# Kernel optimization log

Measured on AMD Instinct MI355X. Metric: run time of the kernel, lower is better.

## Reference

```python
import jax, jax.numpy as jnp
import numpy as np

N_HEADS = 16
ROPE_BASE = 10000.0

def apply_rope(x):
    # x: [B, H, S, D] with D even; interleaved-pair RoPE (torchtune style)
    B, H, S, D = x.shape
    half = D // 2
    inv_freq = 1.0 / (ROPE_BASE ** (jnp.arange(0, half, dtype=jnp.float32) / half))
    angles = jnp.arange(S, dtype=jnp.float32)[:, None] * inv_freq[None, :]  # [S, D/2]
    cos = jnp.cos(angles)[None, None]  # [1,1,S,D/2]
    sin = jnp.sin(angles)[None, None]
    x1 = x[..., 0::2]
    x2 = x[..., 1::2]
    r1 = x1 * cos - x2 * sin
    r2 = x1 * sin + x2 * cos
    return jnp.stack([r1, r2], axis=-1).reshape(B, H, S, D)

def setup_inputs() -> dict:
    key = jax.random.key(0)
    ks = jax.random.split(key, 5)
    B, S, E = 2, 2048, 1024
    d_attn = 1024
    scale = 1.0 / np.sqrt(E)
    x = jax.random.normal(ks[0], (B, S, E), dtype=jnp.float32)
    Wq = jax.random.normal(ks[1], (d_attn, E), dtype=jnp.float32) * scale
    Wk = jax.random.normal(ks[2], (d_attn, E), dtype=jnp.float32) * scale
    Wv = jax.random.normal(ks[3], (d_attn, E), dtype=jnp.float32) * scale
    Wo = jax.random.normal(ks[4], (E, d_attn), dtype=jnp.float32) * scale
    return {"x": x, "Wq": Wq, "Wk": Wk, "Wv": Wv, "Wo": Wo}

def reference(x, Wq, Wk, Wv, Wo):
    B, S, E = x.shape
    d_attn = Wq.shape[0]
    hd = d_attn // N_HEADS
    attn_scale = 1.0 / np.sqrt(d_attn)
    # projections (nn.Linear: x @ W.T), split heads -> [B, H, S, hd]
    q = (x @ Wq.T).reshape(B, S, N_HEADS, hd).transpose(0, 2, 1, 3)
    k = (x @ Wk.T).reshape(B, S, N_HEADS, hd).transpose(0, 2, 1, 3)
    v = (x @ Wv.T).reshape(B, S, N_HEADS, hd).transpose(0, 2, 1, 3)
    q = apply_rope(q)
    k = apply_rope(k)
    scores = jnp.einsum('bhqd,bhkd->bhqk', q, k) * attn_scale  # [B,H,S,S]
    causal = jnp.tril(jnp.ones((S, S), dtype=bool))
    scores = jnp.where(causal[None, None], scores, -jnp.inf)
    probs = jax.nn.softmax(scores, axis=-1)  # dropout is identity in eval
    out = jnp.einsum('bhqk,bhkd->bhqd', probs, v)
    out = out.transpose(0, 2, 1, 3).reshape(B, S, d_attn)
    return out @ Wo.T
```

## Files before the change

### kernel.cpp

```cpp
#include <hip/hip_runtime.h>


typedef float  f32x4  __attribute__((ext_vector_type(4)));
typedef short  short8 __attribute__((ext_vector_type(8)));

#define MFMA16(a,b,c) __builtin_amdgcn_mfma_f32_16x16x32_bf16((a),(b),(c),0,0,0)
#define GLD_LDS16(g, l)                                                        \
  __builtin_amdgcn_global_load_lds(                                            \
      (const __attribute__((address_space(1))) unsigned int*)(g),              \
      (__attribute__((address_space(3))) unsigned int*)(l), 16, 0, 0)

__device__ __forceinline__ unsigned short f2bf(float f) {
  unsigned int x = __float_as_uint(f);
  x += 0x7fffu + ((x >> 16) & 1u);
  return (unsigned short)(x >> 16);
}
__device__ __forceinline__ float bf2f(unsigned short u) {
  return __uint_as_float(((unsigned int)u) << 16);
}

__global__ __launch_bounds__(256) void cvt_all(const float* __restrict__ x,
                                               const float* __restrict__ wq,
                                               const float* __restrict__ wk,
                                               const float* __restrict__ wv,
                                               const float* __restrict__ wo,
                                               ushort* __restrict__ dst) {
  const int i = blockIdx.x * 256 + threadIdx.x;
  const float* src;
  int off;
  if (i < 1048576) { src = x; off = i; }
  else {
    const int j = i - 1048576;
    const int wsel = j >> 18;
    off = j & 262143;
    src = (wsel == 0) ? wq : (wsel == 1) ? wk : (wsel == 2) ? wv : wo;
  }
  const float4 v = ((const float4*)src)[off];
  ushort4 o = make_ushort4(f2bf(v.x), f2bf(v.y), f2bf(v.z), f2bf(v.w));
  ((ushort4*)dst)[i] = o;
}

template<int MODE>
__global__ __launch_bounds__(256) void gemm_bt(const ushort* __restrict__ A,
                                               const ushort* __restrict__ B,
                                               void* __restrict__ Cv,
                                               int K) {
  __shared__ __align__(16) short As[128 * 32];
  __shared__ __align__(16) short Bs[128 * 32];
  const int tid  = threadIdx.x;
  const int lane = tid & 63, w = tid >> 6;
  const int ln   = lane & 15, quad = lane >> 4;
  const int wm   = w >> 1, wn = w & 1;
  const int m0 = blockIdx.y * 128, n0 = blockIdx.x * 128;

  const int srow = lane >> 2;
  const int schk = (lane & 3) * 8;
  const ushort* Ag0 = A + (size_t)(m0 + w * 32      + srow) * K + schk;
  const ushort* Ag1 = A + (size_t)(m0 + w * 32 + 16 + srow) * K + schk;
  const ushort* Bg0 = B + (size_t)(n0 + w * 32      + srow) * K + schk;
  const ushort* Bg1 = B + (size_t)(n0 + w * 32 + 16 + srow) * K + schk;
  short* lA0 = As + (w * 32) * 32;
  short* lA1 = As + (w * 32 + 16) * 32;
  short* lB0 = Bs + (w * 32) * 32;
  short* lB1 = Bs + (w * 32 + 16) * 32;

  int aoff[4], boff[4];
#pragma unroll
  for (int i = 0; i < 4; i++) {
    aoff[i] = (wm * 64 + i * 16 + ln) * 32 + quad * 8;
    boff[i] = (wn * 64 + i * 16 + ln) * 32 + quad * 8;
  }
  f32x4 acc[4][4] = {};

  for (int kt = 0; kt < K; kt += 32) {
    __syncthreads();
    GLD_LDS16(Ag0 + kt, lA0);
    GLD_LDS16(Ag1 + kt, lA1);
    GLD_LDS16(Bg0 + kt, lB0);
    GLD_LDS16(Bg1 + kt, lB1);
    __syncthreads();
    short8 av[4], bv[4];
#pragma unroll
    for (int i = 0; i < 4; i++) av[i] = *(const short8*)&As[aoff[i]];
#pragma unroll
    for (int i = 0; i < 4; i++) bv[i] = *(const short8*)&Bs[boff[i]];
#pragma unroll
    for (int mi = 0; mi < 4; mi++)
#pragma unroll
      for (int ni = 0; ni < 4; ni++)
        acc[mi][ni] = MFMA16(av[mi], bv[ni], acc[mi][ni]);
  }

  if (MODE == 0) {
    ushort* Cq = (ushort*)Cv;
    if (n0 < 2048) {
      ushort* dst = Cq + (n0 < 1024 ? 0 : 4194304);
      const int nbase = (n0 < 1024) ? n0 : n0 - 1024;
#pragma unroll
      for (int mi = 0; mi < 4; mi++) {
        const int row = m0 + wm * 64 + mi * 16 + quad * 4;
#pragma unroll
        for (int ni = 0; ni < 4; ni++) {
          const int col = nbase + wn * 64 + ni * 16 + ln;
#pragma unroll
          for (int r = 0; r < 4; r++)
            dst[(size_t)(row + r) * 1024 + col] = f2bf(acc[mi][ni][r]);
        }
      }
    } else {
      ushort* vt = Cq + 8388608;
#pragma unroll
      for (int mi = 0; mi < 4; mi++) {
        const int sm = m0 + wm * 64 + mi * 16 + quad * 4;
        const int b = sm >> 11, s = sm & 2047;
#pragma unroll
        for (int ni = 0; ni < 4; ni++) {
          const int nv = (n0 - 2048) + wn * 64 + ni * 16 + ln;
          const int bh = b * 16 + (nv >> 6), d = nv & 63;
          ushort4 u = make_ushort4(f2bf(acc[mi][ni][0]), f2bf(acc[mi][ni][1]),
                                   f2bf(acc[mi][ni][2]), f2bf(acc[mi][ni][3]));
          *(ushort4*)&vt[((size_t)bh * 64 + d) * 2048 + s] = u;
        }
      }
    }
  } else {
    float* C = (float*)Cv;
#pragma unroll
    for (int mi = 0; mi < 4; mi++) {
      const int row = m0 + wm * 64 + mi * 16 + quad * 4;
#pragma unroll
      for (int ni = 0; ni < 4; ni++) {
        const int col = n0 + wn * 64 + ni * 16 + ln;
#pragma unroll
        for (int r = 0; r < 4; r++)
          C[(size_t)(row + r) * 1024 + col] = acc[mi][ni][r];
      }
    }
  }
}

__global__ __launch_bounds__(256) void ropek(ushort* __restrict__ qk) {
  const int g  = blockIdx.x * 256 + threadIdx.x;
  const int P0 = g << 2;
  const int mv = P0 >> 9;
  const int s  = mv & 2047;
  const int i0 = P0 & 31;
  const float scale = (mv < 4096) ? 0.04508422002778011f : 1.0f;
  short8 u = *(short8*)&qk[(size_t)P0 * 2];
  short8 ov;
#pragma unroll
  for (int t = 0; t < 4; t++) {
    const float invf = expf(-(float)(i0 + t) * 0.28782313662425574f);
    const float ang  = (float)s * invf;
    float sn, cs;
    sincosf(ang, &sn, &cs);
    const float x1 = bf2f((unsigned short)u[2 * t]);
    const float x2 = bf2f((unsigned short)u[2 * t + 1]);
    ov[2 * t]     = (short)f2bf((x1 * cs - x2 * sn) * scale);
    ov[2 * t + 1] = (short)f2bf((x1 * sn + x2 * cs) * scale);
  }
  *(short8*)&qk[(size_t)P0 * 2] = ov;
}

__global__ __launch_bounds__(256) void attnk(const ushort* __restrict__ q,
                                             const ushort* __restrict__ k,
                                             const ushort* __restrict__ vt,
                                             ushort* __restrict__ ctx) {
  __shared__ __align__(16) short Ks[64 * 72];
  __shared__ __align__(16) short Vs[64 * 72];
  __shared__ __align__(16) short Ps[4 * 16 * 72];
  const int tid  = threadIdx.x;
  const int lane = tid & 63, w = tid >> 6;
  const int ln   = lane & 15, quad = lane >> 4;
  const int x = blockIdx.x, bh = blockIdx.y;
  const int b = bh >> 4, h = bh & 15;
  const int jA = x, jB = 31 - x;
  short* Pw = Ps + w * 1152;

  const size_t qbA = ((size_t)(b * 2048 + jA * 64 + w * 16 + ln)) * 1024 + h * 64;
  const size_t qbB = ((size_t)(b * 2048 + jB * 64 + w * 16 + ln)) * 1024 + h * 64;
  const short8 aqA0 = *(const short8*)&q[qbA + quad * 8];
  const short8 aqA1 = *(const short8*)&q[qbA + 32 + quad * 8];
  const short8 aqB0 = *(const short8*)&q[qbB + quad * 8];
  const short8 aqB1 = *(const short8*)&q[qbB + 32 + quad * 8];

  f32x4 oA[4] = {}, oB[4] = {};
  float lsA[4] = {0.f, 0.f, 0.f, 0.f}, lsB[4] = {0.f, 0.f, 0.f, 0.f};

  const int s0 = tid, s1 = tid + 256;
  const int r0 = s0 >> 3, c0 = (s0 & 7) * 8;
  const int r1 = s1 >> 3, c1 = (s1 & 7) * 8;
  const ushort* kg0 = k  + ((size_t)(b * 2048 + r0)) * 1024 + h * 64 + c0;
  const ushort* kg1 = k  + ((size_t)(b * 2048 + r1)) * 1024 + h * 64 + c1;
  const ushort* vg0 = vt + ((size_t)(bh * 64 + r0)) * 2048 + c0;
  const ushort* vg1 = vt + ((size_t)(bh * 64 + r1)) * 2048 + c1;
  const int wK0 = r0 * 72 + c0, wK1 = r1 * 72 + c1;

  for (int t = 0; t <= jB; t++) {
    __syncthreads();
    *(short8*)&Ks[wK0] = *(const short8*)(kg0 + (size_t)t * 65536);
    *(short8*)&Ks[wK1] = *(const short8*)(kg1 + (size_t)t * 65536);
    *(short8*)&Vs[wK0] = *(const short8*)(vg0 + t * 64);
    *(short8*)&Vs[wK1] = *(const short8*)(vg1 + t * 64);
    __syncthreads();

    const bool actA = (t <= jA);
    f32x4 scA[4], scB[4];
#pragma unroll
    for (int ct = 0; ct < 4; ct++) {
      const short8 bk0 = *(const short8*)&Ks[(ct * 16 + ln) * 72 + quad * 8];
      const short8 bk1 = *(const short8*)&Ks[(ct * 16 + ln) * 72 + 32 + quad * 8];
      f32x4 z = {0.f, 0.f, 0.f, 0.f};
      z = MFMA16(aqB0, bk0, z);
      z = MFMA16(aqB1, bk1, z);
      scB[ct] = z;
      if (actA) {
        f32x4 y = {0.f, 0.f, 0.f, 0.f};
        y = MFMA16(aqA0, bk0, y);
        y = MFMA16(aqA1, bk1, y);
        scA[ct] = y;
      }
    }
    if (t == jB) {
#pragma unroll
      for (int ct = 0; ct < 4; ct++) {
        const int kv = (t << 6) + ct * 16 + ln;
#pragma unroll
        for (int r = 0; r < 4; r++)
          if (kv > jB * 64 + w * 16 + quad * 4 + r) scB[ct][r] = -100000.0f;
      }
    }
    if (actA && t == jA) {
#pragma unroll
      for (int ct = 0; ct < 4; ct++) {
        const int kv = (t << 6) + ct * 16 + ln;
#pragma unroll
        for (int r = 0; r < 4; r++)
          if (kv > jA * 64 + w * 16 + quad * 4 + r) scA[ct][r] = -100000.0f;
      }
    }

    short8 bv0[4], bv1[4];
#pragma unroll
    for (int dt = 0; dt < 4; dt++) {
      bv0[dt] = *(const short8*)&Vs[(dt * 16 + ln) * 72 + quad * 8];
      bv1[dt] = *(const short8*)&Vs[(dt * 16 + ln) * 72 + 32 + quad * 8];
    }

#pragma unroll
    for (int ct = 0; ct < 4; ct++)
#pragma unroll
      for (int r = 0; r < 4; r++) {
        const float p = __builtin_amdgcn_exp2f(scB[ct][r]);
        lsB[r] += p;
        Pw[(quad * 4 + r) * 72 + ct * 16 + ln] = (short)f2bf(p);
      }
    {
      const short8 ap0 = *(const short8*)&Pw[ln * 72 + quad * 8];
      const short8 ap1 = *(const short8*)&Pw[ln * 72 + 32 + quad * 8];
#pragma unroll
      for (int dt = 0; dt < 4; dt++) {
        oB[dt] = MFMA16(ap0, bv0[dt], oB[dt]);
        oB[dt] = MFMA16(ap1, bv1[dt], oB[dt]);
      }
    }
    if (actA) {
#pragma unroll
      for (int ct = 0; ct < 4; ct++)
#pragma unroll
        for (int r = 0; r < 4; r++) {
          const float p = __builtin_amdgcn_exp2f(scA[ct][r]);
          lsA[r] += p;
          Pw[(quad * 4 + r) * 72 + ct * 16 + ln] = (short)f2bf(p);
        }
      const short8 ap0 = *(const short8*)&Pw[ln * 72 + quad * 8];
      const short8 ap1 = *(const short8*)&Pw[ln * 72 + 32 + quad * 8];
#pragma unroll
      for (int dt = 0; dt < 4; dt++) {
        oA[dt] = MFMA16(ap0, bv0[dt], oA[dt]);
        oA[dt] = MFMA16(ap1, bv1[dt], oA[dt]);
      }
    }
  }

#pragma unroll
  for (int off = 1; off < 16; off <<= 1)
#pragma unroll
    for (int r = 0; r < 4; r++) {
      lsA[r] += __shfl_xor(lsA[r], off, 64);
      lsB[r] += __shfl_xor(lsB[r], off, 64);
    }

#pragma unroll
  for (int r = 0; r < 4; r++) {
    const float invA = 1.0f / lsA[r];
    const float invB = 1.0f / lsB[r];
    const int rowA = jA * 64 + w * 16 + quad * 4 + r;
    const int rowB = jB * 64 + w * 16 + quad * 4 + r;
#pragma unroll
    for (int dt = 0; dt < 4; dt++) {
      ctx[((size_t)(b * 2048 + rowA)) * 1024 + h * 64 + dt * 16 + ln] =
          f2bf(oA[dt][r] * invA);
      ctx[((size_t)(b * 2048 + rowB)) * 1024 + h * 64 + dt * 16 + ln] =
          f2bf(oB[dt][r] * invB);
    }
  }
}

extern "C" void kernel_launch(void* const* d_in, const int* in_sizes, int n_in,
                              void* d_out, int out_size, void* d_ws, size_t ws_size,
                              hipStream_t stream) {
  const float* x  = (const float*)d_in[0];
  const float* Wq = (const float*)d_in[1];
  const float* Wk = (const float*)d_in[2];
  const float* Wv = (const float*)d_in[3];
  const float* Wo = (const float*)d_in[4];
  float* out = (float*)d_out;
  char* ws = (char*)d_ws;

  ushort* xb  = (ushort*)(ws);
  ushort* wqb = (ushort*)(ws + (size_t)(8  << 20));
  ushort* qb  = (ushort*)(ws + (size_t)(16 << 20));
  ushort* kb  = (ushort*)(ws + (size_t)(24 << 20));
  ushort* vtb = (ushort*)(ws + (size_t)(32 << 20));
  ushort* ctx = (ushort*)(ws + (size_t)(40 << 20));

  cvt_all<<<8192, 256, 0, stream>>>(x, Wq, Wk, Wv, Wo, xb);
  gemm_bt<0><<<dim3(24, 32), 256, 0, stream>>>(xb, wqb, (void*)qb, 1024);
  ropek<<<4096, 256, 0, stream>>>(qb);
  attnk<<<dim3(16, 32), 256, 0, stream>>>(qb, kb, vtb, ctx);
  gemm_bt<2><<<dim3(8, 32), 256, 0, stream>>>(ctx, wqb + 3145728 , (void*)out, 1024);
}
```

Measured before the change: 205.9 us.

## Split attention KV loop across two wave groups, narrow output GEMM tiles, fast RoPE trig

The attention kernel now runs 512 threads per block. Two groups of four waves each process alternating KV tiles, and their partial outputs and row sums are merged through shared memory at the end, so each block's serial causal loop is roughly half as long. The output projection GEMM uses 64-wide N tiles, which doubles its grid and gives more blocks across the CUs. RoPE switches from expf/sincosf to hardware exp2/sin/cos with explicit range reduction to revolutions, trading a little accuracy for cheaper trig. The cost is a larger shared-memory footprint and an extra reduction step per attention block.

After: 230.7 us. 1.12x slower.

```diff
diff --git a/kernel.cpp b/kernel.cpp
--- a/kernel.cpp
+++ b/kernel.cpp
@@ -40,54 +40,57 @@
   ((ushort4*)dst)[i] = o;
 }
 
-template<int MODE>
+template<int MODE, int BN>
 __global__ __launch_bounds__(256) void gemm_bt(const ushort* __restrict__ A,
                                                const ushort* __restrict__ B,
                                                void* __restrict__ Cv,
                                                int K) {
+  constexpr int NI = BN / 32;
   __shared__ __align__(16) short As[128 * 32];
-  __shared__ __align__(16) short Bs[128 * 32];
+  __shared__ __align__(16) short Bs[BN * 32];
   const int tid  = threadIdx.x;
   const int lane = tid & 63, w = tid >> 6;
   const int ln   = lane & 15, quad = lane >> 4;
   const int wm   = w >> 1, wn = w & 1;
-  const int m0 = blockIdx.y * 128, n0 = blockIdx.x * 128;
+  const int m0 = blockIdx.y * 128, n0 = blockIdx.x * BN;
 
   const int srow = lane >> 2;
   const int schk = (lane & 3) * 8;
   const ushort* Ag0 = A + (size_t)(m0 + w * 32      + srow) * K + schk;
   const ushort* Ag1 = A + (size_t)(m0 + w * 32 + 16 + srow) * K + schk;
-  const ushort* Bg0 = B + (size_t)(n0 + w * 32      + srow) * K + schk;
-  const ushort* Bg1 = B + (size_t)(n0 + w * 32 + 16 + srow) * K + schk;
+  const int brow = (BN == 128) ? w * 32 : w * 16;
+  const ushort* Bg0 = B + (size_t)(n0 + brow + srow) * K + schk;
+  const ushort* Bg1 = B + (size_t)(n0 + brow + 16 + srow) * K + schk;
   short* lA0 = As + (w * 32) * 32;
   short* lA1 = As + (w * 32 + 16) * 32;
-  short* lB0 = Bs + (w * 32) * 32;
-  short* lB1 = Bs + (w * 32 + 16) * 32;
-
-  int aoff[4], boff[4];
-#pragma unroll
-  for (int i = 0; i < 4; i++) {
+  short* lB0 = Bs + brow * 32;
+  short* lB1 = Bs + (brow + 16) * 32;
+
+  int aoff[4], boff[NI];
+#pragma unroll
+  for (int i = 0; i < 4; i++)
     aoff[i] = (wm * 64 + i * 16 + ln) * 32 + quad * 8;
-    boff[i] = (wn * 64 + i * 16 + ln) * 32 + quad * 8;
-  }
-  f32x4 acc[4][4] = {};
+#pragma unroll
+  for (int i = 0; i < NI; i++)
+    boff[i] = (wn * (BN / 2) + i * 16 + ln) * 32 + quad * 8;
+  f32x4 acc[4][NI] = {};
 
   for (int kt = 0; kt < K; kt += 32) {
     __syncthreads();
     GLD_LDS16(Ag0 + kt, lA0);
     GLD_LDS16(Ag1 + kt, lA1);
     GLD_LDS16(Bg0 + kt, lB0);
-    GLD_LDS16(Bg1 + kt, lB1);
+    if (BN == 128) GLD_LDS16(Bg1 + kt, lB1);
     __syncthreads();
-    short8 av[4], bv[4];
+    short8 av[4], bv[NI];
 #pragma unroll
     for (int i = 0; i < 4; i++) av[i] = *(const short8*)&As[aoff[i]];
 #pragma unroll
-    for (int i = 0; i < 4; i++) bv[i] = *(const short8*)&Bs[boff[i]];
+    for (int i = 0; i < NI; i++) bv[i] = *(const short8*)&Bs[boff[i]];
 #pragma unroll
     for (int mi = 0; mi < 4; mi++)
 #pragma unroll
-      for (int ni = 0; ni < 4; ni++)
+      for (int ni = 0; ni < NI; ni++)
         acc[mi][ni] = MFMA16(av[mi], bv[ni], acc[mi][ni]);
   }
 
@@ -100,8 +103,8 @@
       for (int mi = 0; mi < 4; mi++) {
         const int row = m0 + wm * 64 + mi * 16 + quad * 4;
 #pragma unroll
-        for (int ni = 0; ni < 4; ni++) {
-          const int col = nbase + wn * 64 + ni * 16 + ln;
+        for (int ni = 0; ni < NI; ni++) {
+          const int col = nbase + wn * (BN / 2) + ni * 16 + ln;
 #pragma unroll
           for (int r = 0; r < 4; r++)
             dst[(size_t)(row + r) * 1024 + col] = f2bf(acc[mi][ni][r]);
@@ -114,8 +117,8 @@
         const int sm = m0 + wm * 64 + mi * 16 + quad * 4;
         const int b = sm >> 11, s = sm & 2047;
 #pragma unroll
-        for (int ni = 0; ni < 4; ni++) {
-          const int nv = (n0 - 2048) + wn * 64 + ni * 16 + ln;
+        for (int ni = 0; ni < NI; ni++) {
+          const int nv = (n0 - 2048) + wn * (BN / 2) + ni * 16 + ln;
           const int bh = b * 16 + (nv >> 6), d = nv & 63;
           ushort4 u = make_ushort4(f2bf(acc[mi][ni][0]), f2bf(acc[mi][ni][1]),
                                    f2bf(acc[mi][ni][2]), f2bf(acc[mi][ni][3]));
@@ -129,8 +132,8 @@
     for (int mi = 0; mi < 4; mi++) {
       const int row = m0 + wm * 64 + mi * 16 + quad * 4;
 #pragma unroll
-      for (int ni = 0; ni < 4; ni++) {
-        const int col = n0 + wn * 64 + ni * 16 + ln;
+      for (int ni = 0; ni < NI; ni++) {
+        const int col = n0 + wn * (BN / 2) + ni * 16 + ln;
 #pragma unroll
         for (int r = 0; r < 4; r++)
           C[(size_t)(row + r) * 1024 + col] = acc[mi][ni][r];
@@ -146,14 +149,16 @@
   const int s  = mv & 2047;
   const int i0 = P0 & 31;
   const float scale = (mv < 4096) ? 0.04508422002778011f : 1.0f;
+  const float sf = (float)s;
   short8 u = *(short8*)&qk[(size_t)P0 * 2];
   short8 ov;
 #pragma unroll
   for (int t = 0; t < 4; t++) {
-    const float invf = expf(-(float)(i0 + t) * 0.28782313662425574f);
-    const float ang  = (float)s * invf;
-    float sn, cs;
-    sincosf(ang, &sn, &cs);
+    const float invf = __builtin_amdgcn_exp2f(-(float)(i0 + t) * 0.4152410118579865f);
+    const float rev  = sf * invf * 0.15915494309189535f;
+    const float rr   = rev - floorf(rev);
+    const float sn = __builtin_amdgcn_sinf(rr);
+    const float cs = __builtin_amdgcn_cosf(rr);
     const float x1 = bf2f((unsigned short)u[2 * t]);
     const float x2 = bf2f((unsigned short)u[2 * t + 1]);
     ov[2 * t]     = (short)f2bf((x1 * cs - x2 * sn) * scale);
@@ -162,23 +167,31 @@
   *(short8*)&qk[(size_t)P0 * 2] = ov;
 }
 
-__global__ __launch_bounds__(256) void attnk(const ushort* __restrict__ q,
-                                             const ushort* __restrict__ k,
-                                             const ushort* __restrict__ vt,
-                                             ushort* __restrict__ ctx) {
-  __shared__ __align__(16) short Ks[64 * 72];
-  __shared__ __align__(16) short Vs[64 * 72];
-  __shared__ __align__(16) short Ps[4 * 16 * 72];
+__global__ __launch_bounds__(512, 4) void attnk(const ushort* __restrict__ q,
+                                                const ushort* __restrict__ k,
+                                                const ushort* __restrict__ vt,
+                                                ushort* __restrict__ ctx) {
+  __shared__ __align__(16) char smem[55296];
+  short* KsB = (short*)smem;
+  short* VsB = (short*)(smem + 18432);
+  short* PsB = (short*)(smem + 36864);
+  float* OcA = (float*)smem;
+  float* OcB = (float*)(smem + 16384);
+  float* Lc  = (float*)(smem + 32768);
+
   const int tid  = threadIdx.x;
   const int lane = tid & 63, w = tid >> 6;
-  const int ln   = lane & 15, quad = lane >> 4;
+  const int g = w >> 2, wg = w & 3;
+  const int ln = lane & 15, quad = lane >> 4;
   const int x = blockIdx.x, bh = blockIdx.y;
   const int b = bh >> 4, h = bh & 15;
   const int jA = x, jB = 31 - x;
-  short* Pw = Ps + w * 1152;
-
-  const size_t qbA = ((size_t)(b * 2048 + jA * 64 + w * 16 + ln)) * 1024 + h * 64;
-  const size_t qbB = ((size_t)(b * 2048 + jB * 64 + w * 16 + ln)) * 1024 + h * 64;
+  short* Ks = KsB + g * 4608;
+  short* Vs = VsB + g * 4608;
+  short* Pw = PsB + w * 1152;
+
+  const size_t qbA = ((size_t)(b * 2048 + jA * 64 + wg * 16 + ln)) * 1024 + h * 64;
+  const size_t qbB = ((size_t)(b * 2048 + jB * 64 + wg * 16 + ln)) * 1024 + h * 64;
   const short8 aqA0 = *(const short8*)&q[qbA + quad * 8];
   const short8 aqA1 = *(const short8*)&q[qbA + 32 + quad * 8];
   const short8 aqB0 = *(const short8*)&q[qbB + quad * 8];
@@ -187,98 +200,104 @@
   f32x4 oA[4] = {}, oB[4] = {};
   float lsA[4] = {0.f, 0.f, 0.f, 0.f}, lsB[4] = {0.f, 0.f, 0.f, 0.f};
 
-  const int s0 = tid, s1 = tid + 256;
-  const int r0 = s0 >> 3, c0 = (s0 & 7) * 8;
-  const int r1 = s1 >> 3, c1 = (s1 & 7) * 8;
+  const int tg = tid & 255;
+  const int r0 = tg >> 3, c0 = (tg & 7) * 8;
+  const int r1 = r0 + 32, c1 = c0;
   const ushort* kg0 = k  + ((size_t)(b * 2048 + r0)) * 1024 + h * 64 + c0;
   const ushort* kg1 = k  + ((size_t)(b * 2048 + r1)) * 1024 + h * 64 + c1;
   const ushort* vg0 = vt + ((size_t)(bh * 64 + r0)) * 2048 + c0;
   const ushort* vg1 = vt + ((size_t)(bh * 64 + r1)) * 2048 + c1;
   const int wK0 = r0 * 72 + c0, wK1 = r1 * 72 + c1;
 
-  for (int t = 0; t <= jB; t++) {
+  const int nsteps = (jB >> 1) + 1;
+  for (int i = 0; i < nsteps; ++i) {
+    const int t = 2 * i + g;
+    const bool act = (t <= jB);
     __syncthreads();
-    *(short8*)&Ks[wK0] = *(const short8*)(kg0 + (size_t)t * 65536);
-    *(short8*)&Ks[wK1] = *(const short8*)(kg1 + (size_t)t * 65536);
-    *(short8*)&Vs[wK0] = *(const short8*)(vg0 + t * 64);
-    *(short8*)&Vs[wK1] = *(const short8*)(vg1 + t * 64);
+    if (act) {
+      *(short8*)&Ks[wK0] = *(const short8*)(kg0 + (size_t)t * 65536);
+      *(short8*)&Ks[wK1] = *(const short8*)(kg1 + (size_t)t * 65536);
+      *(short8*)&Vs[wK0] = *(const short8*)(vg0 + t * 64);
+      *(short8*)&Vs[wK1] = *(const short8*)(vg1 + t * 64);
+    }
     __syncthreads();
-
-    const bool actA = (t <= jA);
-    f32x4 scA[4], scB[4];
-#pragma unroll
-    for (int ct = 0; ct < 4; ct++) {
-      const short8 bk0 = *(const short8*)&Ks[(ct * 16 + ln) * 72 + quad * 8];
-      const short8 bk1 = *(const short8*)&Ks[(ct * 16 + ln) * 72 + 32 + quad * 8];
-      f32x4 z = {0.f, 0.f, 0.f, 0.f};
-      z = MFMA16(aqB0, bk0, z);
-      z = MFMA16(aqB1, bk1, z);
-      scB[ct] = z;
+    if (act) {
+      const bool actA = (t <= jA);
+      f32x4 scA[4], scB[4];
+#pragma unroll
+      for (int ct = 0; ct < 4; ct++) {
+        const short8 bk0 = *(const short8*)&Ks[(ct * 16 + ln) * 72 + quad * 8];
+        const short8 bk1 = *(const short8*)&Ks[(ct * 16 + ln) * 72 + 32 + quad * 8];
+        f32x4 z = {0.f, 0.f, 0.f, 0.f};
+        z = MFMA16(aqB0, bk0, z);
+        z = MFMA16(aqB1, bk1, z);
+        scB[ct] = z;
+        if (actA) {
+          f32x4 y = {0.f, 0.f, 0.f, 0.f};
+          y = MFMA16(aqA0, bk0, y);
+          y = MFMA16(aqA1, bk1, y);
+          scA[ct] = y;
+        }
+      }
+      if (t == jB) {
+#pragma unroll
+        for (int ct = 0; ct < 4; ct++) {
+          const int kv = (t << 6) + ct * 16 + ln;
+#pragma unroll
+          for (int r = 0; r < 4; r++)
+            if (kv > jB * 64 + wg * 16 + quad * 4 + r) scB[ct][r] = -100000.0f;
+        }
+      }
+      if (actA && t == jA) {
+#pragma unroll
+        for (int ct = 0; ct < 4; ct++) {
+          const int kv = (t << 6) + ct * 16 + ln;
+#pragma unroll
+          for (int r = 0; r < 4; r++)
+            if (kv > jA * 64 + wg * 16 + quad * 4 + r) scA[ct][r] = -100000.0f;
+        }
+      }
+
+      short8 bv0[4], bv1[4];
+#pragma unroll
+      for (int dt = 0; dt < 4; dt++) {
+        bv0[dt] = *(const short8*)&Vs[(dt * 16 + ln) * 72 + quad * 8];
+        bv1[dt] = *(const short8*)&Vs[(dt * 16 + ln) * 72 + 32 + quad * 8];
+      }
+
+#pragma unroll
+      for (int ct = 0; ct < 4; ct++)
+#pragma unroll
+        for (int r = 0; r < 4; r++) {
+          const float p = __builtin_amdgcn_exp2f(scB[ct][r]);
+          lsB[r] += p;
+          Pw[(quad * 4 + r) * 72 + ct * 16 + ln] = (short)f2bf(p);
+        }
+      {
+        const short8 ap0 = *(const short8*)&Pw[ln * 72 + quad * 8];
+        const short8 ap1 = *(const short8*)&Pw[ln * 72 + 32 + quad * 8];
+#pragma unroll
+        for (int dt = 0; dt < 4; dt++) {
+          oB[dt] = MFMA16(ap0, bv0[dt], oB[dt]);
+          oB[dt] = MFMA16(ap1, bv1[dt], oB[dt]);
+        }
+      }
       if (actA) {
-        f32x4 y = {0.f, 0.f, 0.f, 0.f};
-        y = MFMA16(aqA0, bk0, y);
-        y = MFMA16(aqA1, bk1, y);
-        scA[ct] = y;
-      }
-    }
-    if (t == jB) {
-#pragma unroll
-      for (int ct = 0; ct < 4; ct++) {
-        const int kv = (t << 6) + ct * 16 + ln;
-#pragma unroll
-        for (int r = 0; r < 4; r++)
-          if (kv > jB * 64 + w * 16 + quad * 4 + r) scB[ct][r] = -100000.0f;
-      }
-    }
-    if (actA && t == jA) {
-#pragma unroll
-      for (int ct = 0; ct < 4; ct++) {
-        const int kv = (t << 6) + ct * 16 + ln;
-#pragma unroll
-        for (int r = 0; r < 4; r++)
-          if (kv > jA * 64 + w * 16 + quad * 4 + r) scA[ct][r] = -100000.0f;
-      }
-    }
-
-    short8 bv0[4], bv1[4];
-#pragma unroll
-    for (int dt = 0; dt < 4; dt++) {
-      bv0[dt] = *(const short8*)&Vs[(dt * 16 + ln) * 72 + quad * 8];
-      bv1[dt] = *(const short8*)&Vs[(dt * 16 + ln) * 72 + 32 + quad * 8];
-    }
-
-#pragma unroll
-    for (int ct = 0; ct < 4; ct++)
-#pragma unroll
-      for (int r = 0; r < 4; r++) {
-        const float p = __builtin_amdgcn_exp2f(scB[ct][r]);
-        lsB[r] += p;
-        Pw[(quad * 4 + r) * 72 + ct * 16 + ln] = (short)f2bf(p);
-      }
-    {
-      const short8 ap0 = *(const short8*)&Pw[ln * 72 + quad * 8];
-      const short8 ap1 = *(const short8*)&Pw[ln * 72 + 32 + quad * 8];
-#pragma unroll
-      for (int dt = 0; dt < 4; dt++) {
-        oB[dt] = MFMA16(ap0, bv0[dt], oB[dt]);
-        oB[dt] = MFMA16(ap1, bv1[dt], oB[dt]);
-      }
-    }
-    if (actA) {
-#pragma unroll
-      for (int ct = 0; ct < 4; ct++)
-#pragma unroll
-        for (int r = 0; r < 4; r++) {
-          const float p = __builtin_amdgcn_exp2f(scA[ct][r]);
-          lsA[r] += p;
-          Pw[(quad * 4 + r) * 72 + ct * 16 + ln] = (short)f2bf(p);
-        }
-      const short8 ap0 = *(const short8*)&Pw[ln * 72 + quad * 8];
-      const short8 ap1 = *(const short8*)&Pw[ln * 72 + 32 + quad * 8];
-#pragma unroll
-      for (int dt = 0; dt < 4; dt++) {
-        oA[dt] = MFMA16(ap0, bv0[dt], oA[dt]);
-        oA[dt] = MFMA16(ap1, bv1[dt], oA[dt]);
+#pragma unroll
+        for (int ct = 0; ct < 4; ct++)
+#pragma unroll
+          for (int r = 0; r < 4; r++) {
+            const float p = __builtin_amdgcn_exp2f(scA[ct][r]);
+            lsA[r] += p;
+            Pw[(quad * 4 + r) * 72 + ct * 16 + ln] = (short)f2bf(p);
+          }
+        const short8 ap0 = *(const short8*)&Pw[ln * 72 + quad * 8];
+        const short8 ap1 = *(const short8*)&Pw[ln * 72 + 32 + quad * 8];
+#pragma unroll
+        for (int dt = 0; dt < 4; dt++) {
+          oA[dt] = MFMA16(ap0, bv0[dt], oA[dt]);
+          oA[dt] = MFMA16(ap1, bv1[dt], oA[dt]);
+        }
       }
     }
   }
@@ -291,18 +310,38 @@
       lsB[r] += __shfl_xor(lsB[r], off, 64);
     }
 
-#pragma unroll
-  for (int r = 0; r < 4; r++) {
-    const float invA = 1.0f / lsA[r];
-    const float invB = 1.0f / lsB[r];
-    const int rowA = jA * 64 + w * 16 + quad * 4 + r;
-    const int rowB = jB * 64 + w * 16 + quad * 4 + r;
-#pragma unroll
-    for (int dt = 0; dt < 4; dt++) {
-      ctx[((size_t)(b * 2048 + rowA)) * 1024 + h * 64 + dt * 16 + ln] =
-          f2bf(oA[dt][r] * invA);
-      ctx[((size_t)(b * 2048 + rowB)) * 1024 + h * 64 + dt * 16 + ln] =
-          f2bf(oB[dt][r] * invB);
+  __syncthreads();
+  if (g == 1) {
+    const int rl = wg * 16 + quad * 4;
+#pragma unroll
+    for (int dt = 0; dt < 4; dt++)
+#pragma unroll
+      for (int r = 0; r < 4; r++) {
+        OcA[(rl + r) * 64 + dt * 16 + ln] = oA[dt][r];
+        OcB[(rl + r) * 64 + dt * 16 + ln] = oB[dt][r];
+      }
+    if (ln == 0)
+#pragma unroll
+      for (int r = 0; r < 4; r++) {
+        Lc[rl + r]      = lsA[r];
+        Lc[64 + rl + r] = lsB[r];
+      }
+  }
+  __syncthreads();
+  if (g == 0) {
+#pragma unroll
+    for (int r = 0; r < 4; r++) {
+      const int rl = wg * 16 + quad * 4 + r;
+      const float invA = 1.0f / (lsA[r] + Lc[rl]);
+      const float invB = 1.0f / (lsB[r] + Lc[64 + rl]);
+      const int rowA = jA * 64 + rl, rowB = jB * 64 + rl;
+#pragma unroll
+      for (int dt = 0; dt < 4; dt++) {
+        ctx[((size_t)(b * 2048 + rowA)) * 1024 + h * 64 + dt * 16 + ln] =
+            f2bf((oA[dt][r] + OcA[rl * 64 + dt * 16 + ln]) * invA);
+        ctx[((size_t)(b * 2048 + rowB)) * 1024 + h * 64 + dt * 16 + ln] =
+            f2bf((oB[dt][r] + OcB[rl * 64 + dt * 16 + ln]) * invB);
+      }
     }
   }
 }
@@ -326,8 +365,8 @@
   ushort* ctx = (ushort*)(ws + (size_t)(40 << 20));
 
   cvt_all<<<8192, 256, 0, stream>>>(x, Wq, Wk, Wv, Wo, xb);
-  gemm_bt<0><<<dim3(24, 32), 256, 0, stream>>>(xb, wqb, (void*)qb, 1024);
+  gemm_bt<0, 128><<<dim3(24, 32), 256, 0, stream>>>(xb, wqb, (void*)qb, 1024);
   ropek<<<4096, 256, 0, stream>>>(qb);
-  attnk<<<dim3(16, 32), 256, 0, stream>>>(qb, kb, vtb, ctx);
-  gemm_bt<2><<<dim3(8, 32), 256, 0, stream>>>(ctx, wqb + 3145728 , (void*)out, 1024);
-}
+  attnk<<<dim3(16, 32), 512, 0, stream>>>(qb, kb, vtb, ctx);
+  gemm_bt<2, 64><<<dim3(16, 32), 256, 0, stream>>>(ctx, wqb + 3145728 , (void*)out, 1024);
+}
```
